# Kernel tuning notes

Hardware: AMD Instinct MI355X
Metric: run time of the kernel (lower is better)

## Reference

```python
import jax, jax.numpy as jnp
import numpy as np


def setup_inputs() -> dict:
    key = jax.random.key(0)
    ks = jax.random.split(key, 9)
    B, IN, OUT, E, H = 64, 1024, 1024, 8, 8
    return {
        "x": jax.random.normal(ks[0], (B, IN), jnp.float32),
        "weight": jax.random.normal(ks[1], (E, OUT, IN), jnp.float32),
        "align_conv": jax.random.normal(ks[2], (E, E), jnp.float32),
        "W_ih": jax.random.normal(ks[3], (H, 1), jnp.float32),
        "W_hh": jax.random.normal(ks[4], (H, H), jnp.float32),
        "b_ih": jax.random.normal(ks[5], (H,), jnp.float32),
        "b_hh": jax.random.normal(ks[6], (H,), jnp.float32),
        "W_att": jax.random.normal(ks[7], (E, H), jnp.float32),
        "b_att": jax.random.normal(ks[8], (E,), jnp.float32),
    }


def reference(x, weight, align_conv, W_ih, W_hh, b_ih, b_hh, W_att, b_att):
    # attention_up: AdaptiveAvgPool1d(1) over feature dim -> [B, 1]
    pooled = jnp.mean(x, axis=-1, keepdims=True)  # [B, 1]
    # single-step tanh RNN, h0 = 0 (so W_hh contributes 0 in forward)
    h0 = jnp.zeros((x.shape[0], W_hh.shape[0]), x.dtype)
    h = jnp.tanh(pooled @ W_ih.T + h0 @ W_hh.T + b_ih + b_hh)  # [B, 8]
    # attention_down: ReLU -> Linear(8, E) -> Softmax over experts
    att = jax.nn.softmax(jax.nn.relu(h) @ W_att.T + b_att, axis=-1)  # [B, E]
    # align 1x1 conv over the expert axis: [E,E] x [E,out,in] -> [E,out,in]
    w_aligned = jnp.einsum('fe,eoi->foi', align_conv, weight)
    # per-sample fused weight [B, out, in] (the large intermediate)
    fuse_weight = jnp.einsum('be,eoi->boi', att, w_aligned)
    # per-sample matmul: [B,in] x [B,out,in] -> [B,out]
    y = jnp.einsum('bi,boi->bo', x, fuse_weight)
    return y
```

## Files before the change

### kernel.cpp

```cpp
#include <hip/hip_runtime.h>
#include <hip/hip_bf16.h>


typedef short bf16x8 __attribute__((ext_vector_type(8)));
typedef float f32x4 __attribute__((ext_vector_type(4)));

__device__ __forceinline__ unsigned short f2bf(float f) {
    unsigned int u = __builtin_bit_cast(unsigned int, f);
    u += 0x7fffu + ((u >> 16) & 1u);
    return (unsigned short)(u >> 16);
}

#define LDR 40

__global__ __launch_bounds__(256) void zgemm_kernel(
    const float* __restrict__ x,
    const float* __restrict__ w,
    float* __restrict__ z,
    int KC) {
    __shared__ __align__(16) unsigned short xs[64 * LDR];
    __shared__ __align__(16) unsigned short wsld[64 * LDR];

    const int bid = blockIdx.x;
    const int kc  = bid >> 7;
    const int r   = bid & 127;
    const int e   = r >> 4;
    const int ot  = r & 15;
    const int o0  = ot * 64;

    const int t    = threadIdx.x;
    const int lane = t & 63;
    const int wid  = t >> 6;
    const int quad = lane >> 4;
    const int lr   = lane & 15;

    const int kspan = 1024 / KC;
    const int kbase = kc * kspan;
    const int nch   = kspan >> 5;

    f32x4 acc[4];
#pragma unroll
    for (int i = 0; i < 4; ++i) acc[i] = (f32x4){0.f, 0.f, 0.f, 0.f};

    const float4* x4 = (const float4*)x;
    const float4* w4 = (const float4*)w;

    for (int ch = 0; ch < nch; ++ch) {
        const int k0 = kbase + ch * 32;
#pragma unroll
        for (int it = 0; it < 2; ++it) {
            int f   = t + it * 256;
            int row = f >> 3;
            int c4  = f & 7;
            float4 wv = w4[(e * 1024 + o0 + row) * 256 + (k0 >> 2) + c4];
            ushort4 pw;
            pw.x = f2bf(wv.x); pw.y = f2bf(wv.y); pw.z = f2bf(wv.z); pw.w = f2bf(wv.w);
            *(ushort4*)&wsld[row * LDR + c4 * 4] = pw;
            float4 xv = x4[row * 256 + (k0 >> 2) + c4];
            ushort4 px;
            px.x = f2bf(xv.x); px.y = f2bf(xv.y); px.z = f2bf(xv.z); px.w = f2bf(xv.w);
            *(ushort4*)&xs[row * LDR + c4 * 4] = px;
        }
        __syncthreads();
        bf16x8 a = *(const bf16x8*)&xs[(wid * 16 + lr) * LDR + quad * 8];
#pragma unroll
        for (int nt = 0; nt < 4; ++nt) {
            bf16x8 bb = *(const bf16x8*)&wsld[(nt * 16 + lr) * LDR + quad * 8];
            acc[nt] = __builtin_amdgcn_mfma_f32_16x16x32_bf16(a, bb, acc[nt], 0, 0, 0);
        }
        __syncthreads();
    }

    float* zb = z + ((size_t)(kc * 8 + e)) * 64 * 1024;
#pragma unroll
    for (int nt = 0; nt < 4; ++nt) {
        int o = o0 + nt * 16 + lr;
#pragma unroll
        for (int rr = 0; rr < 4; ++rr) {
            int b = wid * 16 + quad * 4 + rr;
            zb[b * 1024 + o] = acc[nt][rr];
        }
    }
}

__global__ __launch_bounds__(256) void combine_kernel(
    const float* __restrict__ x,
    const float* __restrict__ align_conv,
    const float* __restrict__ W_ih,
    const float* __restrict__ b_ih,
    const float* __restrict__ b_hh,
    const float* __restrict__ W_att,
    const float* __restrict__ b_att,
    const float* __restrict__ z,
    float* __restrict__ y,
    int KC) {
    __shared__ float red[4];
    __shared__ float csh[8];

    const int bid = blockIdx.x;
    const int b   = bid >> 2;
    const int oq  = bid & 3;
    const int t    = threadIdx.x;
    const int lane = t & 63;
    const int wid  = t >> 6;

    const float4* x4 = (const float4*)x;
    float4 xv = x4[b * 256 + t];
    float s = xv.x + xv.y + xv.z + xv.w;
#pragma unroll
    for (int off = 32; off > 0; off >>= 1) s += __shfl_down(s, off, 64);
    if (lane == 0) red[wid] = s;
    __syncthreads();

    if (t == 0) {
        float pooled = (red[0] + red[1] + red[2] + red[3]) * (1.0f / 1024.0f);
        float rl[8];
#pragma unroll
        for (int j = 0; j < 8; ++j) {
            float h = tanhf(pooled * W_ih[j] + b_ih[j] + b_hh[j]);
            rl[j] = h > 0.f ? h : 0.f;
        }
        float lg[8];
        float mx = -1e30f;
#pragma unroll
        for (int f = 0; f < 8; ++f) {
            float a = b_att[f];
#pragma unroll
            for (int j = 0; j < 8; ++j) a += rl[j] * W_att[f * 8 + j];
            lg[f] = a;
            mx = fmaxf(mx, a);
        }
        float den = 0.f;
#pragma unroll
        for (int f = 0; f < 8; ++f) { lg[f] = __expf(lg[f] - mx); den += lg[f]; }
        float inv = 1.0f / den;
#pragma unroll
        for (int e = 0; e < 8; ++e) {
            float c = 0.f;
#pragma unroll
            for (int f = 0; f < 8; ++f) c += lg[f] * inv * align_conv[f * 8 + e];
            csh[e] = c;
        }
    }
    __syncthreads();

    const int o = oq * 256 + t;
    float acc = 0.f;
    for (int kc = 0; kc < KC; ++kc) {
#pragma unroll
        for (int e = 0; e < 8; ++e)
            acc += csh[e] * z[(((size_t)(kc * 8 + e) * 64 + b) << 10) + o];
    }
    y[(b << 10) + o] = acc;
}

extern "C" void kernel_launch(void* const* d_in, const int* in_sizes, int n_in,
                              void* d_out, int out_size, void* d_ws, size_t ws_size,
                              hipStream_t stream) {
    const float* x          = (const float*)d_in[0];
    const float* weight     = (const float*)d_in[1];
    const float* align_conv = (const float*)d_in[2];
    const float* W_ih       = (const float*)d_in[3];
    const float* b_ih       = (const float*)d_in[5];
    const float* b_hh       = (const float*)d_in[6];
    const float* W_att      = (const float*)d_in[7];
    const float* b_att      = (const float*)d_in[8];
    float* y = (float*)d_out;
    float* z = (float*)d_ws;

    const size_t slice = (size_t)8 * 64 * 1024 * sizeof(float);
    int KC = (ws_size >= 4 * slice) ? 4 : (ws_size >= 2 * slice) ? 2 : 1;

    zgemm_kernel<<<dim3(128 * KC), dim3(256), 0, stream>>>(x, weight, z, KC);
    combine_kernel<<<dim3(256), dim3(256), 0, stream>>>(x, align_conv, W_ih, b_ih,
                                                        b_hh, W_att, b_att, z, y, KC);
}
```

Before: 104.1 us.

## Fold expert coefficients into GEMM epilogue and split K across 32 chunks

A small coefficient kernel now computes the per-sample expert weights first. The GEMM kernel then loops over all 8 experts, scales each MFMA result by the per-sample coefficient, and accumulates across experts. Work is split over 32 K-chunks × 32 output tiles, which gives 1024 blocks instead of at most 512, and the next expert's weight tile is prefetched through double-buffered LDS. The combine kernel becomes a plain sum over K-chunks, reading 32 partial slices instead of 8×KC, at the cost of a third launch and a fixed workspace need of about 8 MB.

```diff
diff --git a/kernel.cpp b/kernel.cpp
--- a/kernel.cpp
+++ b/kernel.cpp
@@ -13,77 +13,7 @@
 
 #define LDR 40
 
-__global__ __launch_bounds__(256) void zgemm_kernel(
-    const float* __restrict__ x,
-    const float* __restrict__ w,
-    float* __restrict__ z,
-    int KC) {
-    __shared__ __align__(16) unsigned short xs[64 * LDR];
-    __shared__ __align__(16) unsigned short wsld[64 * LDR];
-
-    const int bid = blockIdx.x;
-    const int kc  = bid >> 7;
-    const int r   = bid & 127;
-    const int e   = r >> 4;
-    const int ot  = r & 15;
-    const int o0  = ot * 64;
-
-    const int t    = threadIdx.x;
-    const int lane = t & 63;
-    const int wid  = t >> 6;
-    const int quad = lane >> 4;
-    const int lr   = lane & 15;
-
-    const int kspan = 1024 / KC;
-    const int kbase = kc * kspan;
-    const int nch   = kspan >> 5;
-
-    f32x4 acc[4];
-#pragma unroll
-    for (int i = 0; i < 4; ++i) acc[i] = (f32x4){0.f, 0.f, 0.f, 0.f};
-
-    const float4* x4 = (const float4*)x;
-    const float4* w4 = (const float4*)w;
-
-    for (int ch = 0; ch < nch; ++ch) {
-        const int k0 = kbase + ch * 32;
-#pragma unroll
-        for (int it = 0; it < 2; ++it) {
-            int f   = t + it * 256;
-            int row = f >> 3;
-            int c4  = f & 7;
-            float4 wv = w4[(e * 1024 + o0 + row) * 256 + (k0 >> 2) + c4];
-            ushort4 pw;
-            pw.x = f2bf(wv.x); pw.y = f2bf(wv.y); pw.z = f2bf(wv.z); pw.w = f2bf(wv.w);
-            *(ushort4*)&wsld[row * LDR + c4 * 4] = pw;
-            float4 xv = x4[row * 256 + (k0 >> 2) + c4];
-            ushort4 px;
-            px.x = f2bf(xv.x); px.y = f2bf(xv.y); px.z = f2bf(xv.z); px.w = f2bf(xv.w);
-            *(ushort4*)&xs[row * LDR + c4 * 4] = px;
-        }
-        __syncthreads();
-        bf16x8 a = *(const bf16x8*)&xs[(wid * 16 + lr) * LDR + quad * 8];
-#pragma unroll
-        for (int nt = 0; nt < 4; ++nt) {
-            bf16x8 bb = *(const bf16x8*)&wsld[(nt * 16 + lr) * LDR + quad * 8];
-            acc[nt] = __builtin_amdgcn_mfma_f32_16x16x32_bf16(a, bb, acc[nt], 0, 0, 0);
-        }
-        __syncthreads();
-    }
-
-    float* zb = z + ((size_t)(kc * 8 + e)) * 64 * 1024;
-#pragma unroll
-    for (int nt = 0; nt < 4; ++nt) {
-        int o = o0 + nt * 16 + lr;
-#pragma unroll
-        for (int rr = 0; rr < 4; ++rr) {
-            int b = wid * 16 + quad * 4 + rr;
-            zb[b * 1024 + o] = acc[nt][rr];
-        }
-    }
-}
-
-__global__ __launch_bounds__(256) void combine_kernel(
+__global__ __launch_bounds__(64) void coef_kernel(
     const float* __restrict__ x,
     const float* __restrict__ align_conv,
     const float* __restrict__ W_ih,
@@ -91,29 +21,20 @@
     const float* __restrict__ b_hh,
     const float* __restrict__ W_att,
     const float* __restrict__ b_att,
-    const float* __restrict__ z,
-    float* __restrict__ y,
-    int KC) {
-    __shared__ float red[4];
-    __shared__ float csh[8];
-
-    const int bid = blockIdx.x;
-    const int b   = bid >> 2;
-    const int oq  = bid & 3;
-    const int t    = threadIdx.x;
-    const int lane = t & 63;
-    const int wid  = t >> 6;
-
+    float* __restrict__ ct) {
+    const int b = blockIdx.x;
+    const int lane = threadIdx.x;
     const float4* x4 = (const float4*)x;
-    float4 xv = x4[b * 256 + t];
-    float s = xv.x + xv.y + xv.z + xv.w;
+    float s = 0.f;
+#pragma unroll
+    for (int i = 0; i < 4; ++i) {
+        float4 v = x4[b * 256 + lane + i * 64];
+        s += v.x + v.y + v.z + v.w;
+    }
 #pragma unroll
     for (int off = 32; off > 0; off >>= 1) s += __shfl_down(s, off, 64);
-    if (lane == 0) red[wid] = s;
-    __syncthreads();
-
-    if (t == 0) {
-        float pooled = (red[0] + red[1] + red[2] + red[3]) * (1.0f / 1024.0f);
+    if (lane == 0) {
+        float pooled = s * (1.0f / 1024.0f);
         float rl[8];
 #pragma unroll
         for (int j = 0; j < 8; ++j) {
@@ -139,18 +60,91 @@
             float c = 0.f;
 #pragma unroll
             for (int f = 0; f < 8; ++f) c += lg[f] * inv * align_conv[f * 8 + e];
-            csh[e] = c;
+            ct[e * 64 + b] = c;
         }
     }
+}
+
+__global__ __launch_bounds__(256, 4) void zgemm_kernel(
+    const float* __restrict__ x,
+    const float* __restrict__ w,
+    const float* __restrict__ ct,
+    float* __restrict__ z) {
+    __shared__ __align__(16) unsigned short xs[64 * LDR];
+    __shared__ __align__(16) unsigned short wl[2][32 * LDR];
+    __shared__ float csh[8 * 64];
+
+    const int bid = blockIdx.x;
+    const int ot = bid & 31;
+    const int kc = bid >> 5;
+    const int o0 = ot * 32;
+    const int k0 = kc * 32;
+
+    const int t = threadIdx.x;
+    const int lane = t & 63;
+    const int wid = t >> 6;
+    const int quad = lane >> 4;
+    const int lr = lane & 15;
+
+    const float4* x4 = (const float4*)x;
+    const float4* w4 = (const float4*)w;
+
+#pragma unroll
+    for (int it = 0; it < 2; ++it) {
+        int f = t + it * 256, row = f >> 3, c4 = f & 7;
+        float4 v = x4[row * 256 + (k0 >> 2) + c4];
+        ushort4 p;
+        p.x = f2bf(v.x); p.y = f2bf(v.y); p.z = f2bf(v.z); p.w = f2bf(v.w);
+        *(ushort4*)&xs[row * LDR + c4 * 4] = p;
+    }
+    ((float2*)csh)[t] = ((const float2*)ct)[t];
+    const int wrow = t >> 3, wc4 = t & 7;
+    float4 wreg = w4[(o0 + wrow) * 256 + (k0 >> 2) + wc4];
     __syncthreads();
 
-    const int o = oq * 256 + t;
+    bf16x8 bfrag = *(const bf16x8*)&xs[(wid * 16 + lr) * LDR + quad * 8];
+    const int b = wid * 16 + lr;
+
+    f32x4 accy[2];
+    accy[0] = (f32x4){0.f, 0.f, 0.f, 0.f};
+    accy[1] = (f32x4){0.f, 0.f, 0.f, 0.f};
+    const f32x4 zero = (f32x4){0.f, 0.f, 0.f, 0.f};
+
+    for (int e = 0; e < 8; ++e) {
+        ushort4 p;
+        p.x = f2bf(wreg.x); p.y = f2bf(wreg.y); p.z = f2bf(wreg.z); p.w = f2bf(wreg.w);
+        *(ushort4*)&wl[e & 1][wrow * LDR + wc4 * 4] = p;
+        __syncthreads();
+        if (e < 7) wreg = w4[((e + 1) * 1024 + o0 + wrow) * 256 + (k0 >> 2) + wc4];
+        float cv = csh[e * 64 + b];
+#pragma unroll
+        for (int mt = 0; mt < 2; ++mt) {
+            bf16x8 afrag = *(const bf16x8*)&wl[e & 1][(mt * 16 + lr) * LDR + quad * 8];
+            f32x4 d = __builtin_amdgcn_mfma_f32_16x16x32_bf16(afrag, bfrag, zero, 0, 0, 0);
+#pragma unroll
+            for (int rr = 0; rr < 4; ++rr) accy[mt][rr] += cv * d[rr];
+        }
+    }
+
+#pragma unroll
+    for (int mt = 0; mt < 2; ++mt) {
+        float4 out;
+        out.x = accy[mt][0]; out.y = accy[mt][1]; out.z = accy[mt][2]; out.w = accy[mt][3];
+        *(float4*)&z[(((size_t)(kc * 64 + b)) << 10) + o0 + mt * 16 + quad * 4] = out;
+    }
+}
+
+__global__ __launch_bounds__(256) void combine_kernel(
+    const float* __restrict__ z,
+    float* __restrict__ y) {
+    const int bid = blockIdx.x;
+    const int b = bid >> 2;
+    const int oq = bid & 3;
+    const int o = oq * 256 + threadIdx.x;
     float acc = 0.f;
-    for (int kc = 0; kc < KC; ++kc) {
 #pragma unroll
-        for (int e = 0; e < 8; ++e)
-            acc += csh[e] * z[(((size_t)(kc * 8 + e) * 64 + b) << 10) + o];
-    }
+    for (int kc = 0; kc < 32; ++kc)
+        acc += z[(((size_t)(kc * 64 + b)) << 10) + o];
     y[(b << 10) + o] = acc;
 }
 
@@ -166,12 +160,12 @@
     const float* W_att      = (const float*)d_in[7];
     const float* b_att      = (const float*)d_in[8];
     float* y = (float*)d_out;
-    float* z = (float*)d_ws;
 
-    const size_t slice = (size_t)8 * 64 * 1024 * sizeof(float);
-    int KC = (ws_size >= 4 * slice) ? 4 : (ws_size >= 2 * slice) ? 2 : 1;
+    float* ct = (float*)d_ws;
+    float* z  = (float*)((char*)d_ws + 4096);
 
-    zgemm_kernel<<<dim3(128 * KC), dim3(256), 0, stream>>>(x, weight, z, KC);
-    combine_kernel<<<dim3(256), dim3(256), 0, stream>>>(x, align_conv, W_ih, b_ih,
-                                                        b_hh, W_att, b_att, z, y, KC);
+    coef_kernel<<<dim3(64), dim3(64), 0, stream>>>(x, align_conv, W_ih, b_ih,
+                                                   b_hh, W_att, b_att, ct);
+    zgemm_kernel<<<dim3(1024), dim3(256), 0, stream>>>(x, weight, ct, z);
+    combine_kernel<<<dim3(256), dim3(256), 0, stream>>>(z, y);
 }
```

Result: faster. 98.76 us (-5.1%).
